# Performance work log

Hardware: AMD Instinct MI355X
Metric: run time of the kernel (lower is better)

## Reference

```python
import jax, jax.numpy as jnp
import numpy as np

B, T, D, H = 2, 2048, 512, 8
HD = D // H


def _mha(x, Wi, bi, Wo, bo):
    # torch nn.MultiheadAttention with q=k=v=x, eval mode (no dropout), batch-first math
    b, t, d = x.shape
    qkv = x @ Wi.T + bi                      # (b,t,3D)
    q, k, v = jnp.split(qkv, 3, axis=-1)
    q = q.reshape(b, t, H, HD)
    k = k.reshape(b, t, H, HD)
    v = v.reshape(b, t, H, HD)
    scores = jnp.einsum('bqhd,bkhd->bhqk', q, k) / jnp.sqrt(jnp.float32(HD))
    attn = jax.nn.softmax(scores, axis=-1)   # (b,H,t,t)
    out = jnp.einsum('bhqk,bkhd->bqhd', attn, v).reshape(b, t, d) @ Wo.T + bo
    return out, attn.mean(axis=1)            # weights averaged over heads, torch default


def _block_ids(t, c):
    # importance score is the constant c at every position (grad of sum == ones)
    cum = jnp.cumsum(jnp.full((t,), c, dtype=jnp.float32))
    frac = cum % 1.0
    boundary = (frac < jnp.roll(frac, 1)).astype(jnp.int32)
    return jnp.cumsum(boundary)              # ids in [0, max_blocks]


def _merge(x, ids, m):
    # segment-mean over dynamic blocks; block id 0 (pre-first-boundary) is dropped, as in torch loop i=1..max
    xm = jnp.moveaxis(x, 1, 0)               # (t,b,d)
    sums = jax.ops.segment_sum(xm, ids, num_segments=m + 1)[1:]              # (m,b,d)
    counts = jax.ops.segment_sum(jnp.ones(ids.shape[0], jnp.float32), ids, num_segments=m + 1)[1:]
    merged = sums / (counts[:, None, None] + 1e-10)
    return jnp.moveaxis(merged, 0, 1), counts


def setup_inputs():
    key = jax.random.key(0)
    ks = jax.random.split(key, 12)
    s = 0.02
    d = {'x': jax.random.normal(ks[0], (B, T, D), jnp.float32)}
    for i, n in enumerate(['char', 'block', 'glob']):
        d[n + '_Wi'] = jax.random.normal(ks[1 + 3 * i], (3 * D, D), jnp.float32) * s
        d[n + '_bi'] = jnp.zeros((3 * D,), jnp.float32)
        d[n + '_Wo'] = jax.random.normal(ks[2 + 3 * i], (D, D), jnp.float32) * s
        d[n + '_bo'] = jnp.zeros((D,), jnp.float32)
    d['merge_w'] = jax.random.normal(ks[10], (D,), jnp.float32) * 0.01
    d['merge_b'] = jnp.array([0.37], jnp.float32)
    d['gmerge_w'] = jax.random.normal(ks[11], (D,), jnp.float32) * 0.01
    d['gmerge_b'] = jnp.array([0.41], jnp.float32)
    return d


def reference(x, char_Wi, char_bi, char_Wo, char_bo, block_Wi, block_bi, block_Wo, block_bo,
              glob_Wi, glob_bi, glob_Wo, glob_bo, merge_w, merge_b, gmerge_w, gmerge_b):
    char_out, char_w = _mha(x, char_Wi, char_bi, char_Wo, char_bo)
    c1 = merge_w.sum() + merge_b[0]
    ids1 = _block_ids(T, c1)
    m1 = int(ids1.max())                      # data-independent given weights; concrete in eager
    blocks, cnt1 = _merge(char_out, ids1, m1)
    block_out, block_w = _mha(blocks, block_Wi, block_bi, block_Wo, block_bo)
    c2 = gmerge_w.sum() + gmerge_b[0]
    ids2 = _block_ids(m1, c2)
    m2 = int(ids2.max())
    glob, cnt2 = _merge(block_out, ids2, m2)
    glob_out, glob_w = _mha(glob, glob_Wi, glob_bi, glob_Wo, glob_bo)
    # double repeat_interleave expansion == gather: token t -> char block -> global block
    ids1n = np.asarray(ids1)
    ids2n = np.asarray(ids2)
    token_g = np.where(ids1n >= 1, ids2n[np.maximum(ids1n - 1, 0)], 0)
    tok_idx = np.nonzero(token_g >= 1)[0]
    expanded = glob_out[:, jnp.asarray(token_g[tok_idx] - 1), :]
    return expanded, char_w, block_w, glob_w
```

## Files before the change

### kernel.cpp

```cpp
#include <hip/hip_runtime.h>
#include <cstdint>
#include <cstddef>


#define TB 2
#define TT 2048
#define TD 512
#define TH 8
#define THD 64
#define KC 4

#define MI_M1 0
#define MI_M2 1
#define MI_NTOK 2
#define MI_OFF_CW 3
#define MI_OFF_BW 4
#define MI_OFF_GW 5
#define MI_MCHAR 6
#define MI_MBLOCK 7
#define MI_MGLOB 8
#define MI_SEQC 9
#define MI_SEQB 10
#define MI_SEQG 11

typedef _Float16 half8 __attribute__((ext_vector_type(8)));
typedef _Float16 half4 __attribute__((ext_vector_type(4)));
typedef _Float16 half2_t __attribute__((ext_vector_type(2)));
typedef float floatx4 __attribute__((ext_vector_type(4)));

__device__ __forceinline__ floatx4 mfma16(half8 a, half8 b, floatx4 c) {
  return __builtin_amdgcn_mfma_f32_16x16x32_f16(a, b, c, 0, 0, 0);
}
__device__ __forceinline__ floatx4 mfma16k16(half4 a, half4 b, floatx4 c) {
  return __builtin_amdgcn_mfma_f32_16x16x16f16(a, b, c, 0, 0, 0);
}

__device__ __forceinline__ double fracd(double x) { return x - floor(x); }

__device__ int scan_phase(int n, double c, int* __restrict__ ids,
                          int* __restrict__ startg, float* __restrict__ cntg,
                          int* __restrict__ wsum, int t)
{
  int loc[8];
  const int base = t * 8;
#pragma unroll
  for (int j = 0; j < 8; ++j) {
    const int i = base + j;
    int f = 0;
    if (i < n) {
      const int pidx = (i == 0) ? n : i;
      f = (fracd((double)(i + 1) * c) < fracd((double)pidx * c)) ? 1 : 0;
    }
    loc[j] = f + ((j > 0) ? loc[j - 1] : 0);
  }
  wsum[t] = loc[7];
  __syncthreads();
  for (int off = 1; off < 256; off <<= 1) {
    int u = 0;
    if (t >= off) u = wsum[t - off];
    __syncthreads();
    wsum[t] += u;
    __syncthreads();
  }
  const int excl = wsum[t] - loc[7];
  const int m = wsum[255];
#pragma unroll
  for (int j = 0; j < 8; ++j) {
    const int i = base + j;
    if (i < n) {
      const int id = excl + loc[j];
      ids[i] = id;
      const int f = loc[j] - ((j > 0) ? loc[j - 1] : 0);
      if (f) startg[id - 1] = i;
    }
  }
  __syncthreads();
  for (int j = t; j < m; j += 256)
    cntg[j] = (float)((((j + 1) < m) ? startg[j + 1] : n) - startg[j]);
  __syncthreads();
  return m;
}

__global__ __launch_bounds__(256)
void meta_kernel(const float* __restrict__ mw, const float* __restrict__ mb,
                 const float* __restrict__ gw, const float* __restrict__ gb,
                 int* __restrict__ mi,
                 int* __restrict__ start1, float* __restrict__ cnt1,
                 int* __restrict__ start2, float* __restrict__ cnt2,
                 int* __restrict__ gmap)
{
  __shared__ int ids1[TT];
  __shared__ int ids2[TT];
  __shared__ int wsum[256];
  __shared__ double dsh[256];
  const int t = threadIdx.x;

  double s1 = 0.0, s2 = 0.0;
  for (int i = t; i < TD; i += 256) { s1 += (double)mw[i]; s2 += (double)gw[i]; }
  dsh[t] = s1; __syncthreads();
  for (int off = 128; off > 0; off >>= 1) {
    if (t < off) dsh[t] += dsh[t + off];
    __syncthreads();
  }
  const double c1 = dsh[0] + (double)mb[0];
  __syncthreads();
  dsh[t] = s2; __syncthreads();
  for (int off = 128; off > 0; off >>= 1) {
    if (t < off) dsh[t] += dsh[t + off];
    __syncthreads();
  }
  const double c2 = dsh[0] + (double)gb[0];
  __syncthreads();

  const int m1 = scan_phase(TT, c1, ids1, start1, cnt1, wsum, t);
  const int m2 = scan_phase(m1, c2, ids2, start2, cnt2, wsum, t);

  int i0 = TT;
  if (m1 >= 1 && m2 >= 1) i0 = start1[start2[0]];
  const int ntok = TT - i0;

  if (t == 0) {
    mi[MI_M1] = m1; mi[MI_M2] = m2; mi[MI_NTOK] = ntok;
    const int offcw = TB * ntok * TD;
    mi[MI_OFF_CW] = offcw;
    mi[MI_OFF_BW] = offcw + TB * TT * TT;
    mi[MI_OFF_GW] = offcw + TB * TT * TT + TB * m1 * m1;
    mi[MI_MCHAR] = TB * TT;
    mi[MI_MBLOCK] = TB * m1;
    mi[MI_MGLOB] = TB * m2;
    mi[MI_SEQC] = TT;
    mi[MI_SEQB] = m1;
    mi[MI_SEQG] = m2;
  }
  for (int i = i0 + t; i < TT; i += 256)
    gmap[i - i0] = ids2[ids1[i] - 1] - 1;
}

template <typename OutT, bool SPLIT>
__global__ __launch_bounds__(256)
void gemm_mfma(const float* __restrict__ A, const float* __restrict__ W,
               const float* __restrict__ bias, OutT* __restrict__ C,
               const int* __restrict__ mi, int m_slot, int N)
{
  const int M = mi[m_slot];
  const int bm = blockIdx.y * 128;
  if (bm >= M) return;
  const int bn = blockIdx.x * 64;
  __shared__ _Float16 Ah[128][40];
  __shared__ _Float16 Wh[64][40];
  __shared__ _Float16 Al[SPLIT ? 128 : 1][40];
  __shared__ _Float16 Wl[SPLIT ? 64 : 1][40];

  const int t = threadIdx.x;
  const int wv = t >> 6;
  const int lane = t & 63;
  const int l15 = lane & 15;
  const int quad = lane >> 4;
  const int srowA = t >> 1;
  const int ssegA = (t & 1) * 16;
  const int srowW = t >> 2;
  const int ssegW = (t & 3) * 8;

  floatx4 acc[2][4];
#pragma unroll
  for (int i = 0; i < 2; ++i)
#pragma unroll
    for (int j = 0; j < 4; ++j) acc[i][j] = (floatx4){0.f, 0.f, 0.f, 0.f};

  for (int kk = 0; kk < TD; kk += 32) {
    __syncthreads();
    {
      const int ar = bm + srowA;
#pragma unroll
      for (int u = 0; u < 4; ++u) {
        float4 av = make_float4(0.f, 0.f, 0.f, 0.f);
        if (ar < M) av = *(const float4*)&A[(size_t)ar * TD + kk + ssegA + u * 4];
        const float aa[4] = {av.x, av.y, av.z, av.w};
        half4 hi, lo;
#pragma unroll
        for (int e = 0; e < 4; ++e) {
          const _Float16 h = (_Float16)aa[e];
          hi[e] = h;
          if constexpr (SPLIT) lo[e] = (_Float16)(aa[e] - (float)h);
        }
        *(half4*)&Ah[srowA][ssegA + u * 4] = hi;
        if constexpr (SPLIT) *(half4*)&Al[srowA][ssegA + u * 4] = lo;
      }
#pragma unroll
      for (int u = 0; u < 2; ++u) {
        const float4 wvv = *(const float4*)&W[(size_t)(bn + srowW) * TD + kk + ssegW + u * 4];
        const float ww[4] = {wvv.x, wvv.y, wvv.z, wvv.w};
        half4 hi, lo;
#pragma unroll
        for (int e = 0; e < 4; ++e) {
          const _Float16 h = (_Float16)ww[e];
          hi[e] = h;
          if constexpr (SPLIT) lo[e] = (_Float16)(ww[e] - (float)h);
        }
        *(half4*)&Wh[srowW][ssegW + u * 4] = hi;
        if constexpr (SPLIT) *(half4*)&Wl[srowW][ssegW + u * 4] = lo;
      }
    }
    __syncthreads();
    half8 ah[2], al[2];
#pragma unroll
    for (int mp = 0; mp < 2; ++mp) {
      ah[mp] = *(const half8*)&Ah[wv * 32 + mp * 16 + l15][quad * 8];
      if constexpr (SPLIT) al[mp] = *(const half8*)&Al[wv * 32 + mp * 16 + l15][quad * 8];
    }
#pragma unroll
    for (int np = 0; np < 4; ++np) {
      const half8 bh = *(const half8*)&Wh[np * 16 + l15][quad * 8];
      if constexpr (SPLIT) {
        const half8 bl = *(const half8*)&Wl[np * 16 + l15][quad * 8];
#pragma unroll
        for (int mp = 0; mp < 2; ++mp) {
          acc[mp][np] = mfma16(al[mp], bh, acc[mp][np]);
          acc[mp][np] = mfma16(ah[mp], bl, acc[mp][np]);
          acc[mp][np] = mfma16(ah[mp], bh, acc[mp][np]);
        }
      } else {
#pragma unroll
        for (int mp = 0; mp < 2; ++mp)
          acc[mp][np] = mfma16(ah[mp], bh, acc[mp][np]);
      }
    }
  }
  float bv[4];
#pragma unroll
  for (int np = 0; np < 4; ++np) bv[np] = bias[bn + np * 16 + l15];
#pragma unroll
  for (int mp = 0; mp < 2; ++mp) {
#pragma unroll
    for (int r = 0; r < 4; ++r) {
      const int row = bm + wv * 32 + mp * 16 + quad * 4 + r;
      if (row < M) {
        OutT* cp = &C[(size_t)row * N + bn];
#pragma unroll
        for (int np = 0; np < 4; ++np)
          cp[np * 16 + l15] = (OutT)(acc[mp][np][r] + bv[np]);
      }
    }
  }
}

__global__ __launch_bounds__(256)
void gemm_norm_mfma(const _Float16* __restrict__ Ob, const float* __restrict__ lb,
                    const float* __restrict__ W, const float* __restrict__ bias,
                    float* __restrict__ C, const int* __restrict__ mi,
                    int m_slot, int seq_slot)
{
  const int M = mi[m_slot];
  const int bm = blockIdx.y * 64;
  if (bm >= M) return;
  const int seq = mi[seq_slot];
  const int bn = blockIdx.x * 64;
  __shared__ _Float16 Ah[64][40];
  __shared__ _Float16 Al[64][40];
  __shared__ _Float16 Wh[64][40];
  __shared__ _Float16 Wl[64][40];

  const int t = threadIdx.x;
  const int wv = t >> 6;
  const int lane = t & 63;
  const int l15 = lane & 15;
  const int quad = lane >> 4;
  const int srow = t >> 2;
  const int sseg = (t & 3) * 8;

  const int ar = bm + srow;
  const int ab = (ar >= seq) ? 1 : 0;
  const int aq = ar - ab * seq;

  floatx4 acc[4];
#pragma unroll
  for (int j = 0; j < 4; ++j) acc[j] = (floatx4){0.f, 0.f, 0.f, 0.f};

  for (int kk = 0; kk < TD; kk += 32) {
    __syncthreads();
    {
      float aa[8] = {0.f, 0.f, 0.f, 0.f, 0.f, 0.f, 0.f, 0.f};
      if (ar < M) {
        const size_t off = (size_t)ar * TD + kk + sseg;
#pragma unroll
        for (int z = 0; z < KC; ++z) {
          const half8 hv = *(const half8*)&Ob[(size_t)z * 2097152 + off];
#pragma unroll
          for (int e = 0; e < 8; ++e) aa[e] += (float)hv[e];
        }
        const int h = kk >> 6;
        const size_t lidx = ((size_t)(ab * TH + h)) * 2048 + aq;
        float lt = 0.f;
#pragma unroll
        for (int z = 0; z < KC; ++z) lt += lb[(size_t)z * 32768 + lidx];
        const float linv = 1.f / lt;
#pragma unroll
        for (int e = 0; e < 8; ++e) aa[e] *= linv;
      }
      half8 hi, lo;
#pragma unroll
      for (int e = 0; e < 8; ++e) {
        const _Float16 h = (_Float16)aa[e];
        hi[e] = h; lo[e] = (_Float16)(aa[e] - (float)h);
      }
      *(half8*)&Ah[srow][sseg] = hi;
      *(half8*)&Al[srow][sseg] = lo;

      const float4 w0 = *(const float4*)&W[(size_t)(bn + srow) * TD + kk + sseg];
      const float4 w1 = *(const float4*)&W[(size_t)(bn + srow) * TD + kk + sseg + 4];
      const float ww[8] = {w0.x, w0.y, w0.z, w0.w, w1.x, w1.y, w1.z, w1.w};
      half8 whi, wlo;
#pragma unroll
      for (int e = 0; e < 8; ++e) {
        const _Float16 h = (_Float16)ww[e];
        whi[e] = h; wlo[e] = (_Float16)(ww[e] - (float)h);
      }
      *(half8*)&Wh[srow][sseg] = whi;
      *(half8*)&Wl[srow][sseg] = wlo;
    }
    __syncthreads();
    const half8 ah = *(const half8*)&Ah[wv * 16 + l15][quad * 8];
    const half8 al = *(const half8*)&Al[wv * 16 + l15][quad * 8];
#pragma unroll
    for (int np = 0; np < 4; ++np) {
      const half8 bh = *(const half8*)&Wh[np * 16 + l15][quad * 8];
      const half8 bl = *(const half8*)&Wl[np * 16 + l15][quad * 8];
      acc[np] = mfma16(al, bh, acc[np]);
      acc[np] = mfma16(ah, bl, acc[np]);
      acc[np] = mfma16(ah, bh, acc[np]);
    }
  }
  float bv[4];
#pragma unroll
  for (int np = 0; np < 4; ++np) bv[np] = bias[bn + np * 16 + l15];
#pragma unroll
  for (int r = 0; r < 4; ++r) {
    const int row = bm + wv * 16 + quad * 4 + r;
    if (row < M) {
      float* cp = &C[(size_t)row * 512 + bn];
#pragma unroll
      for (int np = 0; np < 4; ++np)
        cp[np * 16 + l15] = acc[np][r] + bv[np];
    }
  }
}

__global__ __launch_bounds__(256)
void attn1_mfma(const _Float16* __restrict__ qkv,
                float* __restrict__ lbase, _Float16* __restrict__ Obase,
                const int* __restrict__ mi, int seq_slot)
{
  const int seq = mi[seq_slot];
  const int q0 = blockIdx.x * 128;
  if (q0 >= seq) return;
  const int b = blockIdx.y >> 3, h = blockIdx.y & 7;
  const int z = blockIdx.z;
  float* lP = lbase + (size_t)z * 32768;
  _Float16* oP = Obase + (size_t)z * 2097152;
  const int t = threadIdx.x;
  const int wv = t >> 6;
  const int lane = t & 63;
  const int l15 = lane & 15;
  const int quad = lane >> 4;

  __shared__ __align__(16) char smem_raw[18432];
  _Float16 (*Kf)[72] = (_Float16 (*)[72])smem_raw;
  _Float16 (*Vt)[72] = (_Float16 (*)[72])(smem_raw + 9216);
  float    (*Ot)[68] = (float (*)[68])smem_raw;

  half8 qB[2][2];
#pragma unroll
  for (int mp = 0; mp < 2; ++mp) {
    const int qrow = q0 + wv * 32 + mp * 16 + l15;
#pragma unroll
    for (int c = 0; c < 2; ++c) {
      half8 v = {};
      if (qrow < seq)
        v = *(const half8*)&qkv[((size_t)(b * seq + qrow)) * 1536 + h * 64 + c * 32 + quad * 8];
      qB[mp][c] = v;
    }
  }
  half4 onesA;
#pragma unroll
  for (int j = 0; j < 4; ++j) onesA[j] = (_Float16)1.0f;

  floatx4 oacc[2][4];
#pragma unroll
  for (int i = 0; i < 2; ++i)
#pragma unroll
    for (int j = 0; j < 4; ++j) oacc[i][j] = (floatx4){0.f, 0.f, 0.f, 0.f};
  floatx4 lacc[2] = {(floatx4){0.f, 0.f, 0.f, 0.f}, (floatx4){0.f, 0.f, 0.f, 0.f}};

  const int nkt = (seq + 63) >> 6;
  const int nkc = (nkt + KC - 1) / KC;
  const int kt_beg = z * nkc;
  const int kt_end = min(kt_beg + nkc, nkt);

  for (int kt = kt_beg; kt < kt_end; ++kt) {
    const int k0 = kt * 64;
    __syncthreads();
    {
      const int row = t >> 2;
      const int seg = (t & 3) * 16;
      const int kg = k0 + row;
      half8 v0 = {}, v1 = {};
      if (kg < seq) {
        const _Float16* base = &qkv[((size_t)(b * seq + kg)) * 1536 + 512 + h * 64 + seg];
        v0 = *(const half8*)base;
        v1 = *(const half8*)(base + 8);
      }
      *(half8*)&Kf[row][seg] = v0;
      *(half8*)&Kf[row][seg + 8] = v1;
    }
    {
      const int tp = lane & 31;
      const int dsel = lane >> 5;
      const int dbase = wv * 16 + dsel * 8;
      const int kg0 = k0 + tp * 2;
      half8 vA = {}, vB = {};
      if (kg0 < seq)
        vA = *(const half8*)&qkv[((size_t)(b * seq + kg0)) * 1536 + 1024 + h * 64 + dbase];
      if (kg0 + 1 < seq)
        vB = *(const half8*)&qkv[((size_t)(b * seq + kg0 + 1)) * 1536 + 1024 + h * 64 + dbase];
#pragma unroll
      for (int j = 0; j < 8; ++j) {
        half2_t pk; pk[0] = vA[j]; pk[1] = vB[j];
        *(half2_t*)&Vt[dbase + j][tp * 2] = pk;
      }
    }
    __syncthreads();

#pragma unroll
    for (int p = 0; p < 4; ++p) {
      floatx4 sT[2] = {(floatx4){0.f, 0.f, 0.f, 0.f}, (floatx4){0.f, 0.f, 0.f, 0.f}};
#pragma unroll
      for (int c = 0; c < 2; ++c) {
        const half8 kA = *(const half8*)&Kf[p * 16 + l15][c * 32 + quad * 8];
#pragma unroll
        for (int mp = 0; mp < 2; ++mp)
          sT[mp] = mfma16(kA, qB[mp][c], sT[mp]);
      }
      half4 vA[4];
#pragma unroll
      for (int dblk = 0; dblk < 4; ++dblk)
        vA[dblk] = *(const half4*)&Vt[dblk * 16 + l15][p * 16 + quad * 4];
      const int kg = k0 + p * 16 + quad * 4;
#pragma unroll
      for (int mp = 0; mp < 2; ++mp) {
        half4 eB;
#pragma unroll
        for (int r = 0; r < 4; ++r) {
          const float e = (kg + r < seq) ? __expf(sT[mp][r] * 0.125f) : 0.f;
          eB[r] = (_Float16)e;
        }
        lacc[mp] = mfma16k16(onesA, eB, lacc[mp]);
#pragma unroll
        for (int dblk = 0; dblk < 4; ++dblk)
          oacc[mp][dblk] = mfma16k16(vA[dblk], eB, oacc[mp][dblk]);
      }
    }
  }

  __syncthreads();

#pragma unroll
  for (int mp = 0; mp < 2; ++mp) {
#pragma unroll
    for (int dblk = 0; dblk < 4; ++dblk)
      *(floatx4*)&Ot[wv * 16 + l15][dblk * 16 + quad * 4] = oacc[mp][dblk];
    const int ql = lane >> 2;
    const int dseg = (lane & 3) * 4;
    const int qg = q0 + wv * 32 + mp * 16 + ql;
    if (qg < seq) {
      _Float16* op = &oP[((size_t)(b * seq + qg)) * 512 + h * 64];
#pragma unroll
      for (int u = 0; u < 4; ++u) {
        const float4 v = *(const float4*)&Ot[wv * 16 + ql][u * 16 + dseg];
        half4 hv;
        hv[0] = (_Float16)v.x; hv[1] = (_Float16)v.y;
        hv[2] = (_Float16)v.z; hv[3] = (_Float16)v.w;
        *(half4*)(op + u * 16 + dseg) = hv;
      }
    }
    if (quad == 0) {
      const int qg2 = q0 + wv * 32 + mp * 16 + l15;
      if (qg2 < seq)
        lP[((size_t)(b * TH + h)) * 2048 + qg2] = lacc[mp][0];
    }
  }
}

__global__ __launch_bounds__(256)
void attn2_mfma(const _Float16* __restrict__ qkv,
                const float* __restrict__ lb,
                float* __restrict__ outb, const int* __restrict__ mi,
                int seq_slot, int off_slot)
{
  const int seq = mi[seq_slot];
  const int q0 = blockIdx.y * 64;
  const int k0 = blockIdx.x * 128;
  if (q0 >= seq || k0 >= seq) return;
  const int b = blockIdx.z;
  const int woff = mi[off_slot];
  float* wout = outb + (size_t)woff + (size_t)b * seq * seq;

  __shared__ _Float16 Qs[64][72];
  __shared__ _Float16 Ksh[128][72];
  __shared__ float Linv[64];

  const int t = threadIdx.x;
  const int wv = t >> 6;
  const int lane = t & 63;
  const int l15 = lane & 15;
  const int quad = lane >> 4;
  const int srowQ = t >> 2;
  const int ssegQ = (t & 3) * 16;
  const int srowK = t >> 1;
  const int ssegK = (t & 1) * 32;

  floatx4 acc[8];
#pragma unroll
  for (int j = 0; j < 8; ++j) acc[j] = (floatx4){0.f, 0.f, 0.f, 0.f};

  for (int h = 0; h < TH; ++h) {
    __syncthreads();
    {
      const int qr = q0 + srowQ;
      half8 q0v = {}, q1v = {};
      if (qr < seq) {
        const _Float16* base = &qkv[((size_t)(b * seq + qr)) * 1536 + h * 64 + ssegQ];
        q0v = *(const half8*)base;
        q1v = *(const half8*)(base + 8);
      }
      *(half8*)&Qs[srowQ][ssegQ] = q0v;
      *(half8*)&Qs[srowQ][ssegQ + 8] = q1v;

      const int kr = k0 + srowK;
#pragma unroll
      for (int u = 0; u < 4; ++u) {
        half8 kv = {};
        if (kr < seq)
          kv = *(const half8*)&qkv[((size_t)(b * seq + kr)) * 1536 + 512 + h * 64 + ssegK + u * 8];
        *(half8*)&Ksh[srowK][ssegK + u * 8] = kv;
      }
      if (t < 64) {
        float lv = 1.f;
        if (q0 + t < seq) {
          const size_t lidx = ((size_t)(b * TH + h)) * 2048 + q0 + t;
          float lt = 0.f;
#pragma unroll
          for (int z = 0; z < KC; ++z) lt += lb[(size_t)z * 32768 + lidx];
          lv = lt;
        }
        Linv[t] = 1.f / lv;
      }
    }
    __syncthreads();

    half8 af[2];
#pragma unroll
    for (int c = 0; c < 2; ++c)
      af[c] = *(const half8*)&Qs[wv * 16 + l15][c * 32 + quad * 8];
    float lv[4];
#pragma unroll
    for (int r = 0; r < 4; ++r)
      lv[r] = Linv[wv * 16 + quad * 4 + r];

#pragma unroll
    for (int np = 0; np < 8; ++np) {
      half8 bf[2];
#pragma unroll
      for (int c = 0; c < 2; ++c)
        bf[c] = *(const half8*)&Ksh[np * 16 + l15][c * 32 + quad * 8];
      floatx4 s = (floatx4){0.f, 0.f, 0.f, 0.f};
      s = mfma16(af[0], bf[0], s);
      s = mfma16(af[1], bf[1], s);
#pragma unroll
      for (int r = 0; r < 4; ++r)
        acc[np][r] += __expf(s[r] * 0.125f) * lv[r];
    }
  }

#pragma unroll
  for (int r = 0; r < 4; ++r) {
    const int qg = q0 + wv * 16 + quad * 4 + r;
    if (qg >= seq) continue;
    float* rowp = wout + (size_t)qg * seq;
#pragma unroll
    for (int np = 0; np < 8; ++np) {
      const int col = k0 + np * 16 + l15;
      if (col < seq) rowp[col] = acc[np][r] * 0.125f;
    }
  }
}

__global__ __launch_bounds__(256)
void merge_kernel(const float* __restrict__ src, float* __restrict__ dst,
                  const int* __restrict__ start, const float* __restrict__ cnt,
                  const int* __restrict__ mi, int seqin_slot, int seqout_slot)
{
  const int j = blockIdx.x;
  const int b = blockIdx.y;
  const int seqo = mi[seqout_slot];
  if (j >= seqo) return;
  const int seqi = mi[seqin_slot];
  const int s = start[j];
  const float cf = cnt[j];
  const int n = (int)cf;
  const int d0 = threadIdx.x * 2;
  float s0 = 0.f, s1 = 0.f;
  const float* p = &src[((size_t)b * seqi + s) * TD + d0];
  for (int i = 0; i < n; ++i) {
    const float2 v = *(const float2*)p;
    s0 += v.x; s1 += v.y;
    p += TD;
  }
  const float inv = 1.f / (cf + 1e-10f);
  float2 o; o.x = s0 * inv; o.y = s1 * inv;
  *(float2*)&dst[((size_t)b * seqo + j) * TD + d0] = o;
}

__global__ __launch_bounds__(256)
void expand_kernel(const float* __restrict__ gout, float* __restrict__ dout,
                   const int* __restrict__ gmap, const int* __restrict__ mi)
{
  const int j = blockIdx.x;
  const int b = blockIdx.y;
  const int ntok = mi[MI_NTOK];
  if (j >= ntok) return;
  const int m2 = mi[MI_M2];
  const int g = gmap[j];
  const int d0 = threadIdx.x * 2;
  const float2 v = *(const float2*)&gout[((size_t)b * m2 + g) * TD + d0];
  *(float2*)&dout[((size_t)b * ntok + j) * TD + d0] = v;
}

extern "C" void kernel_launch(void* const* d_in, const int* in_sizes, int n_in,
                              void* d_out, int out_size, void* d_ws, size_t ws_size,
                              hipStream_t stream)
{
  const float* x   = (const float*)d_in[0];
  const float* cWi = (const float*)d_in[1];
  const float* cbi = (const float*)d_in[2];
  const float* cWo = (const float*)d_in[3];
  const float* cbo = (const float*)d_in[4];
  const float* bWi = (const float*)d_in[5];
  const float* bbi = (const float*)d_in[6];
  const float* bWo = (const float*)d_in[7];
  const float* bbo = (const float*)d_in[8];
  const float* gWi = (const float*)d_in[9];
  const float* gbi = (const float*)d_in[10];
  const float* gWo = (const float*)d_in[11];
  const float* gbo = (const float*)d_in[12];
  const float* mw  = (const float*)d_in[13];
  const float* mbv = (const float*)d_in[14];
  const float* gw  = (const float*)d_in[15];
  const float* gbv = (const float*)d_in[16];
  float* outf = (float*)d_out;

  char* wsb = (char*)d_ws;
  int*   mi     = (int*)(wsb);
  int*   start1 = (int*)(wsb + 1024);
  float* cnt1   = (float*)(wsb + 1024 + 8192);
  int*   start2 = (int*)(wsb + 1024 + 2 * 8192);
  float* cnt2   = (float*)(wsb + 1024 + 3 * 8192);
  int*   gmap   = (int*)(wsb + 1024 + 4 * 8192);
  float* lbase  = (float*)(wsb + 65536);
  _Float16* qkv = (_Float16*)(wsb + 655360);
  _Float16* Obase = (_Float16*)(wsb + 655360 + 12582912);
  float* stg_o  = (float*)(wsb + 655360 + 12582912 + (size_t)KC * 4194304);
  float* stg_m  = stg_o + 2097152;

  const dim3 blk(256);

  meta_kernel<<<dim3(1), blk, 0, stream>>>(mw, mbv, gw, gbv, mi, start1, cnt1, start2, cnt2, gmap);

  gemm_mfma<_Float16, false><<<dim3(24, 32), blk, 0, stream>>>(x, cWi, cbi, qkv, mi, MI_MCHAR, 1536);
  attn1_mfma<<<dim3(16, 16, KC), blk, 0, stream>>>(qkv, lbase, Obase, mi, MI_SEQC);
  attn2_mfma<<<dim3(16, 32, 2), blk, 0, stream>>>(qkv, lbase, outf, mi, MI_SEQC, MI_OFF_CW);
  gemm_norm_mfma<<<dim3(8, 64), blk, 0, stream>>>(Obase, lbase, cWo, cbo, stg_o, mi, MI_MCHAR, MI_SEQC);
  merge_kernel<<<dim3(2048, 2), blk, 0, stream>>>(stg_o, stg_m, start1, cnt1, mi, MI_SEQC, MI_SEQB);

  gemm_mfma<_Float16, false><<<dim3(24, 32), blk, 0, stream>>>(stg_m, bWi, bbi, qkv, mi, MI_MBLOCK, 1536);
  attn1_mfma<<<dim3(16, 16, KC), blk, 0, stream>>>(qkv, lbase, Obase, mi, MI_SEQB);
  attn2_mfma<<<dim3(16, 32, 2), blk, 0, stream>>>(qkv, lbase, outf, mi, MI_SEQB, MI_OFF_BW);
  gemm_norm_mfma<<<dim3(8, 64), blk, 0, stream>>>(Obase, lbase, bWo, bbo, stg_o, mi, MI_MBLOCK, MI_SEQB);
  merge_kernel<<<dim3(2048, 2), blk, 0, stream>>>(stg_o, stg_m, start2, cnt2, mi, MI_SEQB, MI_SEQG);

  gemm_mfma<_Float16, false><<<dim3(24, 32), blk, 0, stream>>>(stg_m, gWi, gbi, qkv, mi, MI_MGLOB, 1536);
  attn1_mfma<<<dim3(16, 16, KC), blk, 0, stream>>>(qkv, lbase, Obase, mi, MI_SEQG);
  attn2_mfma<<<dim3(16, 32, 2), blk, 0, stream>>>(qkv, lbase, outf, mi, MI_SEQG, MI_OFF_GW);
  gemm_norm_mfma<<<dim3(8, 64), blk, 0, stream>>>(Obase, lbase, gWo, gbo, stg_o, mi, MI_MGLOB, MI_SEQG);
  expand_kernel<<<dim3(2048, 2), blk, 0, stream>>>(stg_o, outf, gmap, mi);

  (void)in_sizes; (void)n_in; (void)out_size; (void)ws_size;
}
```

Measured before the change: 396.4 us.

## Double-buffer shared tiles with register prefetch across GEMM and attention kernels

Converts the GEMM, normalized-output GEMM, and both attention kernels to double-buffered shared memory. Each kernel prefetches the next tile's global loads into registers while computing on the current one, and uses a single barrier per iteration that waits only on LDS traffic, not outstanding global loads. attn2 now loads Q fragments directly into registers, precomputes the normalizers for all heads up front, and attn1 skips the mask check on full key tiles. This hides global-load latency at the cost of doubled LDS and extra registers, which may reduce occupancy.

```diff
diff --git a/kernel.cpp b/kernel.cpp
--- a/kernel.cpp
+++ b/kernel.cpp
@@ -35,6 +35,11 @@
   return __builtin_amdgcn_mfma_f32_16x16x16f16(a, b, c, 0, 0, 0);
 }
 
+__device__ __forceinline__ void barrier_nodrain() {
+  asm volatile("s_waitcnt lgkmcnt(0)" ::: "memory");
+  __builtin_amdgcn_s_barrier();
+}
+
 __device__ __forceinline__ double fracd(double x) { return x - floor(x); }
 
 __device__ int scan_phase(int n, double c, int* __restrict__ ids,
@@ -136,20 +141,17 @@
     gmap[i - i0] = ids2[ids1[i] - 1] - 1;
 }
 
-template <typename OutT, bool SPLIT>
 __global__ __launch_bounds__(256)
 void gemm_mfma(const float* __restrict__ A, const float* __restrict__ W,
-               const float* __restrict__ bias, OutT* __restrict__ C,
+               const float* __restrict__ bias, _Float16* __restrict__ C,
                const int* __restrict__ mi, int m_slot, int N)
 {
   const int M = mi[m_slot];
   const int bm = blockIdx.y * 128;
   if (bm >= M) return;
   const int bn = blockIdx.x * 64;
-  __shared__ _Float16 Ah[128][40];
-  __shared__ _Float16 Wh[64][40];
-  __shared__ _Float16 Al[SPLIT ? 128 : 1][40];
-  __shared__ _Float16 Wl[SPLIT ? 64 : 1][40];
+  __shared__ _Float16 Ah[2][128][40];
+  __shared__ _Float16 Wh[2][64][40];
 
   const int t = threadIdx.x;
   const int wv = t >> 6;
@@ -160,6 +162,9 @@
   const int ssegA = (t & 1) * 16;
   const int srowW = t >> 2;
   const int ssegW = (t & 3) * 8;
+  const int ar = bm + srowA;
+  const size_t abase = (size_t)ar * TD + ssegA;
+  const size_t wbase = (size_t)(bn + srowW) * TD + ssegW;
 
   floatx4 acc[2][4];
 #pragma unroll
@@ -167,63 +172,54 @@
 #pragma unroll
     for (int j = 0; j < 4; ++j) acc[i][j] = (floatx4){0.f, 0.f, 0.f, 0.f};
 
-  for (int kk = 0; kk < TD; kk += 32) {
-    __syncthreads();
-    {
-      const int ar = bm + srowA;
-#pragma unroll
-      for (int u = 0; u < 4; ++u) {
-        float4 av = make_float4(0.f, 0.f, 0.f, 0.f);
-        if (ar < M) av = *(const float4*)&A[(size_t)ar * TD + kk + ssegA + u * 4];
-        const float aa[4] = {av.x, av.y, av.z, av.w};
-        half4 hi, lo;
-#pragma unroll
-        for (int e = 0; e < 4; ++e) {
-          const _Float16 h = (_Float16)aa[e];
-          hi[e] = h;
-          if constexpr (SPLIT) lo[e] = (_Float16)(aa[e] - (float)h);
-        }
-        *(half4*)&Ah[srowA][ssegA + u * 4] = hi;
-        if constexpr (SPLIT) *(half4*)&Al[srowA][ssegA + u * 4] = lo;
-      }
-#pragma unroll
-      for (int u = 0; u < 2; ++u) {
-        const float4 wvv = *(const float4*)&W[(size_t)(bn + srowW) * TD + kk + ssegW + u * 4];
-        const float ww[4] = {wvv.x, wvv.y, wvv.z, wvv.w};
-        half4 hi, lo;
-#pragma unroll
-        for (int e = 0; e < 4; ++e) {
-          const _Float16 h = (_Float16)ww[e];
-          hi[e] = h;
-          if constexpr (SPLIT) lo[e] = (_Float16)(ww[e] - (float)h);
-        }
-        *(half4*)&Wh[srowW][ssegW + u * 4] = hi;
-        if constexpr (SPLIT) *(half4*)&Wl[srowW][ssegW + u * 4] = lo;
-      }
-    }
-    __syncthreads();
-    half8 ah[2], al[2];
-#pragma unroll
-    for (int mp = 0; mp < 2; ++mp) {
-      ah[mp] = *(const half8*)&Ah[wv * 32 + mp * 16 + l15][quad * 8];
-      if constexpr (SPLIT) al[mp] = *(const half8*)&Al[wv * 32 + mp * 16 + l15][quad * 8];
-    }
+  float4 pa[4];
+  float4 pw[2];
+
+  auto LOADT = [&](int kk) {
+#pragma unroll
+    for (int u = 0; u < 4; ++u) {
+      pa[u] = make_float4(0.f, 0.f, 0.f, 0.f);
+      if (ar < M) pa[u] = *(const float4*)&A[abase + kk + u * 4];
+    }
+#pragma unroll
+    for (int u = 0; u < 2; ++u)
+      pw[u] = *(const float4*)&W[wbase + kk + u * 4];
+  };
+  auto WRITET = [&](int buf) {
+#pragma unroll
+    for (int u = 0; u < 4; ++u) {
+      const float aa[4] = {pa[u].x, pa[u].y, pa[u].z, pa[u].w};
+      half4 hv;
+#pragma unroll
+      for (int e = 0; e < 4; ++e) hv[e] = (_Float16)aa[e];
+      *(half4*)&Ah[buf][srowA][ssegA + u * 4] = hv;
+    }
+#pragma unroll
+    for (int u = 0; u < 2; ++u) {
+      const float ww[4] = {pw[u].x, pw[u].y, pw[u].z, pw[u].w};
+      half4 hv;
+#pragma unroll
+      for (int e = 0; e < 4; ++e) hv[e] = (_Float16)ww[e];
+      *(half4*)&Wh[buf][srowW][ssegW + u * 4] = hv;
+    }
+  };
+
+  LOADT(0);
+  for (int it = 0; it < TD / 32; ++it) {
+    const int buf = it & 1;
+    WRITET(buf);
+    if (it + 1 < TD / 32) LOADT((it + 1) * 32);
+    barrier_nodrain();
+    half8 ah[2];
+#pragma unroll
+    for (int mp = 0; mp < 2; ++mp)
+      ah[mp] = *(const half8*)&Ah[buf][wv * 32 + mp * 16 + l15][quad * 8];
 #pragma unroll
     for (int np = 0; np < 4; ++np) {
-      const half8 bh = *(const half8*)&Wh[np * 16 + l15][quad * 8];
-      if constexpr (SPLIT) {
-        const half8 bl = *(const half8*)&Wl[np * 16 + l15][quad * 8];
-#pragma unroll
-        for (int mp = 0; mp < 2; ++mp) {
-          acc[mp][np] = mfma16(al[mp], bh, acc[mp][np]);
-          acc[mp][np] = mfma16(ah[mp], bl, acc[mp][np]);
-          acc[mp][np] = mfma16(ah[mp], bh, acc[mp][np]);
-        }
-      } else {
-#pragma unroll
-        for (int mp = 0; mp < 2; ++mp)
-          acc[mp][np] = mfma16(ah[mp], bh, acc[mp][np]);
-      }
+      const half8 bh = *(const half8*)&Wh[buf][np * 16 + l15][quad * 8];
+#pragma unroll
+      for (int mp = 0; mp < 2; ++mp)
+        acc[mp][np] = mfma16(ah[mp], bh, acc[mp][np]);
     }
   }
   float bv[4];
@@ -235,10 +231,10 @@
     for (int r = 0; r < 4; ++r) {
       const int row = bm + wv * 32 + mp * 16 + quad * 4 + r;
       if (row < M) {
-        OutT* cp = &C[(size_t)row * N + bn];
+        _Float16* cp = &C[(size_t)row * N + bn];
 #pragma unroll
         for (int np = 0; np < 4; ++np)
-          cp[np * 16 + l15] = (OutT)(acc[mp][np][r] + bv[np]);
+          cp[np * 16 + l15] = (_Float16)(acc[mp][np][r] + bv[np]);
       }
     }
   }
@@ -255,10 +251,10 @@
   if (bm >= M) return;
   const int seq = mi[seq_slot];
   const int bn = blockIdx.x * 64;
-  __shared__ _Float16 Ah[64][40];
-  __shared__ _Float16 Al[64][40];
-  __shared__ _Float16 Wh[64][40];
-  __shared__ _Float16 Wl[64][40];
+  __shared__ _Float16 Ah[2][64][40];
+  __shared__ _Float16 Al[2][64][40];
+  __shared__ _Float16 Wh[2][64][40];
+  __shared__ _Float16 Wl[2][64][40];
 
   const int t = threadIdx.x;
   const int wv = t >> 6;
@@ -276,55 +272,72 @@
 #pragma unroll
   for (int j = 0; j < 4; ++j) acc[j] = (floatx4){0.f, 0.f, 0.f, 0.f};
 
-  for (int kk = 0; kk < TD; kk += 32) {
-    __syncthreads();
-    {
-      float aa[8] = {0.f, 0.f, 0.f, 0.f, 0.f, 0.f, 0.f, 0.f};
-      if (ar < M) {
-        const size_t off = (size_t)ar * TD + kk + sseg;
-#pragma unroll
-        for (int z = 0; z < KC; ++z) {
-          const half8 hv = *(const half8*)&Ob[(size_t)z * 2097152 + off];
-#pragma unroll
-          for (int e = 0; e < 8; ++e) aa[e] += (float)hv[e];
-        }
-        const int h = kk >> 6;
-        const size_t lidx = ((size_t)(ab * TH + h)) * 2048 + aq;
-        float lt = 0.f;
-#pragma unroll
-        for (int z = 0; z < KC; ++z) lt += lb[(size_t)z * 32768 + lidx];
-        const float linv = 1.f / lt;
-#pragma unroll
-        for (int e = 0; e < 8; ++e) aa[e] *= linv;
-      }
-      half8 hi, lo;
-#pragma unroll
-      for (int e = 0; e < 8; ++e) {
-        const _Float16 h = (_Float16)aa[e];
-        hi[e] = h; lo[e] = (_Float16)(aa[e] - (float)h);
-      }
-      *(half8*)&Ah[srow][sseg] = hi;
-      *(half8*)&Al[srow][sseg] = lo;
-
-      const float4 w0 = *(const float4*)&W[(size_t)(bn + srow) * TD + kk + sseg];
-      const float4 w1 = *(const float4*)&W[(size_t)(bn + srow) * TD + kk + sseg + 4];
-      const float ww[8] = {w0.x, w0.y, w0.z, w0.w, w1.x, w1.y, w1.z, w1.w};
-      half8 whi, wlo;
-#pragma unroll
-      for (int e = 0; e < 8; ++e) {
-        const _Float16 h = (_Float16)ww[e];
-        whi[e] = h; wlo[e] = (_Float16)(ww[e] - (float)h);
-      }
-      *(half8*)&Wh[srow][sseg] = whi;
-      *(half8*)&Wl[srow][sseg] = wlo;
-    }
-    __syncthreads();
-    const half8 ah = *(const half8*)&Ah[wv * 16 + l15][quad * 8];
-    const half8 al = *(const half8*)&Al[wv * 16 + l15][quad * 8];
+  const half8 h8z = {};
+  half8 pOb[KC];
+  float plb[KC];
+  float4 pw0, pw1;
+
+  auto LOADT = [&](int kk) {
+    if (ar < M) {
+      const size_t off = (size_t)ar * TD + kk + sseg;
+#pragma unroll
+      for (int z = 0; z < KC; ++z)
+        pOb[z] = *(const half8*)&Ob[(size_t)z * 2097152 + off];
+      const int h = kk >> 6;
+      const size_t lidx = ((size_t)(ab * TH + h)) * 2048 + aq;
+#pragma unroll
+      for (int z = 0; z < KC; ++z) plb[z] = lb[(size_t)z * 32768 + lidx];
+    } else {
+#pragma unroll
+      for (int z = 0; z < KC; ++z) { pOb[z] = h8z; plb[z] = 1.f; }
+    }
+    pw0 = *(const float4*)&W[(size_t)(bn + srow) * TD + kk + sseg];
+    pw1 = *(const float4*)&W[(size_t)(bn + srow) * TD + kk + sseg + 4];
+  };
+  auto WRITET = [&](int buf) {
+    float aa[8] = {0.f, 0.f, 0.f, 0.f, 0.f, 0.f, 0.f, 0.f};
+    if (ar < M) {
+#pragma unroll
+      for (int z = 0; z < KC; ++z)
+#pragma unroll
+        for (int e = 0; e < 8; ++e) aa[e] += (float)pOb[z][e];
+      const float lt = plb[0] + plb[1] + plb[2] + plb[3];
+      const float linv = 1.f / lt;
+#pragma unroll
+      for (int e = 0; e < 8; ++e) aa[e] *= linv;
+    }
+    half8 hi, lo;
+#pragma unroll
+    for (int e = 0; e < 8; ++e) {
+      const _Float16 h = (_Float16)aa[e];
+      hi[e] = h; lo[e] = (_Float16)(aa[e] - (float)h);
+    }
+    *(half8*)&Ah[buf][srow][sseg] = hi;
+    *(half8*)&Al[buf][srow][sseg] = lo;
+
+    const float ww[8] = {pw0.x, pw0.y, pw0.z, pw0.w, pw1.x, pw1.y, pw1.z, pw1.w};
+    half8 whi, wlo;
+#pragma unroll
+    for (int e = 0; e < 8; ++e) {
+      const _Float16 h = (_Float16)ww[e];
+      whi[e] = h; wlo[e] = (_Float16)(ww[e] - (float)h);
+    }
+    *(half8*)&Wh[buf][srow][sseg] = whi;
+    *(half8*)&Wl[buf][srow][sseg] = wlo;
+  };
+
+  LOADT(0);
+  for (int it = 0; it < TD / 32; ++it) {
+    const int buf = it & 1;
+    WRITET(buf);
+    if (it + 1 < TD / 32) LOADT((it + 1) * 32);
+    barrier_nodrain();
+    const half8 ah = *(const half8*)&Ah[buf][wv * 16 + l15][quad * 8];
+    const half8 al = *(const half8*)&Al[buf][wv * 16 + l15][quad * 8];
 #pragma unroll
     for (int np = 0; np < 4; ++np) {
-      const half8 bh = *(const half8*)&Wh[np * 16 + l15][quad * 8];
-      const half8 bl = *(const half8*)&Wl[np * 16 + l15][quad * 8];
+      const half8 bh = *(const half8*)&Wh[buf][np * 16 + l15][quad * 8];
+      const half8 bl = *(const half8*)&Wl[buf][np * 16 + l15][quad * 8];
       acc[np] = mfma16(al, bh, acc[np]);
       acc[np] = mfma16(ah, bl, acc[np]);
       acc[np] = mfma16(ah, bh, acc[np]);
@@ -363,10 +376,8 @@
   const int l15 = lane & 15;
   const int quad = lane >> 4;
 
-  __shared__ __align__(16) char smem_raw[18432];
-  _Float16 (*Kf)[72] = (_Float16 (*)[72])smem_raw;
-  _Float16 (*Vt)[72] = (_Float16 (*)[72])(smem_raw + 9216);
-  float    (*Ot)[68] = (float (*)[68])smem_raw;
+  __shared__ __align__(16) char smem_raw[36864];
+  float (*Ot)[68] = (float (*)[68])smem_raw;
 
   half8 qB[2][2];
 #pragma unroll
@@ -396,40 +407,49 @@
   const int kt_beg = z * nkc;
   const int kt_end = min(kt_beg + nkc, nkt);
 
+  const int krow = t >> 2;
+  const int kseg = (t & 3) * 16;
+  const int tp = lane & 31;
+  const int dsel = lane >> 5;
+  const int dbase = wv * 16 + dsel * 8;
+
+  const half8 h8z = {};
+  half8 pk0, pk1, pva, pvb;
+
+  auto LOADKV = [&](int kt) {
+    const int k0 = kt * 64;
+    pk0 = h8z; pk1 = h8z; pva = h8z; pvb = h8z;
+    const int kg = k0 + krow;
+    if (kg < seq) {
+      const _Float16* base = &qkv[((size_t)(b * seq + kg)) * 1536 + 512 + h * 64 + kseg];
+      pk0 = *(const half8*)base;
+      pk1 = *(const half8*)(base + 8);
+    }
+    const int kg0 = k0 + tp * 2;
+    if (kg0 < seq)
+      pva = *(const half8*)&qkv[((size_t)(b * seq + kg0)) * 1536 + 1024 + h * 64 + dbase];
+    if (kg0 + 1 < seq)
+      pvb = *(const half8*)&qkv[((size_t)(b * seq + kg0 + 1)) * 1536 + 1024 + h * 64 + dbase];
+  };
+
+  LOADKV(kt_beg);
   for (int kt = kt_beg; kt < kt_end; ++kt) {
+    char* sb = smem_raw + (size_t)((kt - kt_beg) & 1) * 18432;
+    _Float16 (*Kf)[72] = (_Float16 (*)[72])sb;
+    _Float16 (*Vt)[72] = (_Float16 (*)[72])(sb + 9216);
+
+    *(half8*)&Kf[krow][kseg] = pk0;
+    *(half8*)&Kf[krow][kseg + 8] = pk1;
+#pragma unroll
+    for (int j = 0; j < 8; ++j) {
+      half2_t pkk; pkk[0] = pva[j]; pkk[1] = pvb[j];
+      *(half2_t*)&Vt[dbase + j][tp * 2] = pkk;
+    }
+    if (kt + 1 < kt_end) LOADKV(kt + 1);
+    barrier_nodrain();
+
     const int k0 = kt * 64;
-    __syncthreads();
-    {
-      const int row = t >> 2;
-      const int seg = (t & 3) * 16;
-      const int kg = k0 + row;
-      half8 v0 = {}, v1 = {};
-      if (kg < seq) {
-        const _Float16* base = &qkv[((size_t)(b * seq + kg)) * 1536 + 512 + h * 64 + seg];
-        v0 = *(const half8*)base;
-        v1 = *(const half8*)(base + 8);
-      }
-      *(half8*)&Kf[row][seg] = v0;
-      *(half8*)&Kf[row][seg + 8] = v1;
-    }
-    {
-      const int tp = lane & 31;
-      const int dsel = lane >> 5;
-      const int dbase = wv * 16 + dsel * 8;
-      const int kg0 = k0 + tp * 2;
-      half8 vA = {}, vB = {};
-      if (kg0 < seq)
-        vA = *(const half8*)&qkv[((size_t)(b * seq + kg0)) * 1536 + 1024 + h * 64 + dbase];
-      if (kg0 + 1 < seq)
-        vB = *(const half8*)&qkv[((size_t)(b * seq + kg0 + 1)) * 1536 + 1024 + h * 64 + dbase];
-#pragma unroll
-      for (int j = 0; j < 8; ++j) {
-        half2_t pk; pk[0] = vA[j]; pk[1] = vB[j];
-        *(half2_t*)&Vt[dbase + j][tp * 2] = pk;
-      }
-    }
-    __syncthreads();
-
+    const bool kfull = (k0 + 64 <= seq);
 #pragma unroll
     for (int p = 0; p < 4; ++p) {
       floatx4 sT[2] = {(floatx4){0.f, 0.f, 0.f, 0.f}, (floatx4){0.f, 0.f, 0.f, 0.f}};
@@ -448,10 +468,16 @@
 #pragma unroll
       for (int mp = 0; mp < 2; ++mp) {
         half4 eB;
-#pragma unroll
-        for (int r = 0; r < 4; ++r) {
-          const float e = (kg + r < seq) ? __expf(sT[mp][r] * 0.125f) : 0.f;
-          eB[r] = (_Float16)e;
+        if (kfull) {
+#pragma unroll
+          for (int r = 0; r < 4; ++r)
+            eB[r] = (_Float16)__expf(sT[mp][r] * 0.125f);
+        } else {
+#pragma unroll
+          for (int r = 0; r < 4; ++r) {
+            const float e = (kg + r < seq) ? __expf(sT[mp][r] * 0.125f) : 0.f;
+            eB[r] = (_Float16)e;
+          }
         }
         lacc[mp] = mfma16k16(onesA, eB, lacc[mp]);
 #pragma unroll
@@ -504,81 +530,88 @@
   const int woff = mi[off_slot];
   float* wout = outb + (size_t)woff + (size_t)b * seq * seq;
 
-  __shared__ _Float16 Qs[64][72];
-  __shared__ _Float16 Ksh[128][72];
-  __shared__ float Linv[64];
+  __shared__ _Float16 Ksh[2][128][72];
+  __shared__ float Linv8[TH][64];
 
   const int t = threadIdx.x;
   const int wv = t >> 6;
   const int lane = t & 63;
   const int l15 = lane & 15;
   const int quad = lane >> 4;
-  const int srowQ = t >> 2;
-  const int ssegQ = (t & 3) * 16;
   const int srowK = t >> 1;
   const int ssegK = (t & 1) * 32;
 
+  for (int i = t; i < TH * 64; i += 256) {
+    const int hh = i >> 6;
+    const int qq = i & 63;
+    float lv = 1.f;
+    if (q0 + qq < seq) {
+      const size_t lidx = ((size_t)(b * TH + hh)) * 2048 + q0 + qq;
+      float lt = 0.f;
+#pragma unroll
+      for (int zz = 0; zz < KC; ++zz) lt += lb[(size_t)zz * 32768 + lidx];
+      lv = lt;
+    }
+    Linv8[hh][qq] = 1.f / lv;
+  }
+
   floatx4 acc[8];
 #pragma unroll
   for (int j = 0; j < 8; ++j) acc[j] = (floatx4){0.f, 0.f, 0.f, 0.f};
 
+  const int qr = q0 + wv * 16 + l15;
+  const int kr = k0 + srowK;
+  const bool qok = (qr < seq);
+  const bool kok = (kr < seq);
+  const size_t qoff = (size_t)(b * seq + qr) * 1536 + quad * 8;
+  const size_t koff = (size_t)(b * seq + kr) * 1536 + 512 + ssegK;
+
+  const half8 h8z = {};
+  half8 pk[4];
+  half8 qcur0, qcur1, qnxt0, qnxt1;
+
+  auto LOADK = [&](int h) {
+#pragma unroll
+    for (int u = 0; u < 4; ++u) {
+      pk[u] = h8z;
+      if (kok) pk[u] = *(const half8*)&qkv[koff + h * 64 + u * 8];
+    }
+  };
+  auto LOADQ = [&](int h, half8& d0, half8& d1) {
+    d0 = h8z; d1 = h8z;
+    if (qok) {
+      d0 = *(const half8*)&qkv[qoff + h * 64];
+      d1 = *(const half8*)&qkv[qoff + h * 64 + 32];
+    }
+  };
+
+  LOADK(0);
+  LOADQ(0, qcur0, qcur1);
   for (int h = 0; h < TH; ++h) {
-    __syncthreads();
-    {
-      const int qr = q0 + srowQ;
-      half8 q0v = {}, q1v = {};
-      if (qr < seq) {
-        const _Float16* base = &qkv[((size_t)(b * seq + qr)) * 1536 + h * 64 + ssegQ];
-        q0v = *(const half8*)base;
-        q1v = *(const half8*)(base + 8);
-      }
-      *(half8*)&Qs[srowQ][ssegQ] = q0v;
-      *(half8*)&Qs[srowQ][ssegQ + 8] = q1v;
-
-      const int kr = k0 + srowK;
-#pragma unroll
-      for (int u = 0; u < 4; ++u) {
-        half8 kv = {};
-        if (kr < seq)
-          kv = *(const half8*)&qkv[((size_t)(b * seq + kr)) * 1536 + 512 + h * 64 + ssegK + u * 8];
-        *(half8*)&Ksh[srowK][ssegK + u * 8] = kv;
-      }
-      if (t < 64) {
-        float lv = 1.f;
-        if (q0 + t < seq) {
-          const size_t lidx = ((size_t)(b * TH + h)) * 2048 + q0 + t;
-          float lt = 0.f;
-#pragma unroll
-          for (int z = 0; z < KC; ++z) lt += lb[(size_t)z * 32768 + lidx];
-          lv = lt;
-        }
-        Linv[t] = 1.f / lv;
-      }
-    }
-    __syncthreads();
-
-    half8 af[2];
-#pragma unroll
-    for (int c = 0; c < 2; ++c)
-      af[c] = *(const half8*)&Qs[wv * 16 + l15][c * 32 + quad * 8];
+    const int buf = h & 1;
+#pragma unroll
+    for (int u = 0; u < 4; ++u)
+      *(half8*)&Ksh[buf][srowK][ssegK + u * 8] = pk[u];
+    if (h + 1 < TH) { LOADK(h + 1); LOADQ(h + 1, qnxt0, qnxt1); }
+    barrier_nodrain();
+
     float lv[4];
 #pragma unroll
     for (int r = 0; r < 4; ++r)
-      lv[r] = Linv[wv * 16 + quad * 4 + r];
+      lv[r] = Linv8[h][wv * 16 + quad * 4 + r];
 
 #pragma unroll
     for (int np = 0; np < 8; ++np) {
-      half8 bf[2];
-#pragma unroll
-      for (int c = 0; c < 2; ++c)
-        bf[c] = *(const half8*)&Ksh[np * 16 + l15][c * 32 + quad * 8];
+      const half8 bf0 = *(const half8*)&Ksh[buf][np * 16 + l15][quad * 8];
+      const half8 bf1 = *(const half8*)&Ksh[buf][np * 16 + l15][32 + quad * 8];
       floatx4 s = (floatx4){0.f, 0.f, 0.f, 0.f};
-      s = mfma16(af[0], bf[0], s);
-      s = mfma16(af[1], bf[1], s);
+      s = mfma16(qcur0, bf0, s);
+      s = mfma16(qcur1, bf1, s);
 #pragma unroll
       for (int r = 0; r < 4; ++r)
         acc[np][r] += __expf(s[r] * 0.125f) * lv[r];
     }
+    qcur0 = qnxt0; qcur1 = qnxt1;
   }
 
 #pragma unroll
@@ -675,19 +708,19 @@
 
   meta_kernel<<<dim3(1), blk, 0, stream>>>(mw, mbv, gw, gbv, mi, start1, cnt1, start2, cnt2, gmap);
 
-  gemm_mfma<_Float16, false><<<dim3(24, 32), blk, 0, stream>>>(x, cWi, cbi, qkv, mi, MI_MCHAR, 1536);
+  gemm_mfma<<<dim3(24, 32), blk, 0, stream>>>(x, cWi, cbi, qkv, mi, MI_MCHAR, 1536);
   attn1_mfma<<<dim3(16, 16, KC), blk, 0, stream>>>(qkv, lbase, Obase, mi, MI_SEQC);
   attn2_mfma<<<dim3(16, 32, 2), blk, 0, stream>>>(qkv, lbase, outf, mi, MI_SEQC, MI_OFF_CW);
   gemm_norm_mfma<<<dim3(8, 64), blk, 0, stream>>>(Obase, lbase, cWo, cbo, stg_o, mi, MI_MCHAR, MI_SEQC);
   merge_kernel<<<dim3(2048, 2), blk, 0, stream>>>(stg_o, stg_m, start1, cnt1, mi, MI_SEQC, MI_SEQB);
 
-  gemm_mfma<_Float16, false><<<dim3(24, 32), blk, 0, stream>>>(stg_m, bWi, bbi, qkv, mi, MI_MBLOCK, 1536);
+  gemm_mfma<<<dim3(24, 32), blk, 0, stream>>>(stg_m, bWi, bbi, qkv, mi, MI_MBLOCK, 1536);
   attn1_mfma<<<dim3(16, 16, KC), blk, 0, stream>>>(qkv, lbase, Obase, mi, MI_SEQB);
   attn2_mfma<<<dim3(16, 32, 2), blk, 0, stream>>>(qkv, lbase, outf, mi, MI_SEQB, MI_OFF_BW);
   gemm_norm_mfma<<<dim3(8, 64), blk, 0, stream>>>(Obase, lbase, bWo, bbo, stg_o, mi, MI_MBLOCK, MI_SEQB);
   merge_kernel<<<dim3(2048, 2), blk, 0, stream>>>(stg_o, stg_m, start2, cnt2, mi, MI_SEQB, MI_SEQG);
 
-  gemm_mfma<_Float16, false><<<dim3(24, 32), blk, 0, stream>>>(stg_m, gWi, gbi, qkv, mi, MI_MGLOB, 1536);
+  gemm_mfma<<<dim3(24, 32), blk, 0, stream>>>(stg_m, gWi, gbi, qkv, mi, MI_MGLOB, 1536);
   attn1_mfma<<<dim3(16, 16, KC), blk, 0, stream>>>(qkv, lbase, Obase, mi, MI_SEQG);
   attn2_mfma<<<dim3(16, 32, 2), blk, 0, stream>>>(qkv, lbase, outf, mi, MI_SEQG, MI_OFF_GW);
   gemm_norm_mfma<<<dim3(8, 64), blk, 0, stream>>>(Obase, lbase, gWo, gbo, stg_o, mi, MI_MGLOB, MI_SEQG);
```

Result: faster. 349.2 us (-11.9%).
